# Kernel tuning notes

Measured on AMD Instinct MI355X. Metric: run time of the kernel, lower is better.

Reference implementation:

```python
import jax, jax.numpy as jnp
import numpy as np

N_USERS = 100000
N_MOVIES = 50000
EMB_DIM = 64
N_EDGES = 5000000


def setup_inputs() -> dict:
    key = jax.random.key(0)
    k1, k2, k3 = jax.random.split(key, 3)
    N = N_USERS + N_MOVIES
    edge_index = jax.random.randint(k1, (2, N_EDGES), 0, N, dtype=jnp.int64)
    user_emb = 0.1 * jax.random.normal(k2, (N_USERS, EMB_DIM), dtype=jnp.float32)
    movie_emb = 0.1 * jax.random.normal(k3, (N_MOVIES, EMB_DIM), dtype=jnp.float32)
    return {"edge_index": edge_index, "n_layers": 3,
            "user_emb": user_emb, "movie_emb": movie_emb}


def reference(edge_index, n_layers, user_emb, movie_emb):
    n_users = user_emb.shape[0]
    N = n_users + movie_emb.shape[0]
    x = jnp.concatenate([user_emb, movie_emb], axis=0)  # [N, D]

    row, col = edge_index[0], edge_index[1]  # source -> target
    # gcn_norm without self-loops (LGConv default): deg from target (col)
    deg = jnp.zeros((N,), x.dtype).at[col].add(1.0)
    dis = jnp.where(deg > 0, jax.lax.rsqrt(jnp.maximum(deg, 1.0)), 0.0)
    norm = dis[row] * dis[col]  # [E]

    acc = x
    total = x
    for _ in range(n_layers):
        msg = acc[row] * norm[:, None]            # [E, D] gather + scale
        acc = jax.ops.segment_sum(msg, col, num_segments=N)  # scatter-add
        total = total + acc
    final = total / (n_layers + 1)                # mean over layers 0..K
    return final[:n_users], final[n_users:]
```

## Files before the change

kernel.cpp:

```cpp
#include <hip/hip_runtime.h>

typedef _Float16 half_t;
typedef _Float16 half2_t __attribute__((ext_vector_type(2)));
union pk_u { unsigned int u; half2_t h; };

#define EMB 64
#define NLAYERS 3
#define BSH2 9
#define BW2 512
#define NB2MAX 512
#define GSPREAD 32
#define CAP 20480
#define EGCAP 34816
#define P1_BATCH 4096
#define P1_TH 512
#define P1_EPT 8
#define BINTH 1024

__device__ inline void scan_512w(const int* __restrict__ in, int* __restrict__ lstart,
                                 int* __restrict__ pair) {
    int t = threadIdx.x;
    int a0 = 0, a1 = 0;
    if (t < 256) { a0 = in[2 * t]; a1 = in[2 * t + 1]; pair[t] = a0 + a1; }
    __syncthreads();
    for (int off = 1; off < 256; off <<= 1) {
        int u = 0;
        if (t < 256 && t >= off) u = pair[t - off];
        __syncthreads();
        if (t < 256) pair[t] += u;
        __syncthreads();
    }
    if (t < 256) {
        lstart[2 * t]     = pair[t] - a0 - a1;
        lstart[2 * t + 1] = pair[t] - a1;
    }
    __syncthreads();
}

__global__ __launch_bounds__(512) void part_kernel(
        const int* __restrict__ row, const int* __restrict__ col,
        int* __restrict__ gcount, int* __restrict__ tmp, int E, int nb2) {
    __shared__ int hist[NB2MAX];
    __shared__ int lstart[NB2MAX];
    __shared__ int gbase[NB2MAX];
    __shared__ int pair[256];
    __shared__ int srec[P1_BATCH];
    __shared__ unsigned short sbuck[P1_BATCH];

    int base = blockIdx.x * P1_BATCH;
    int nE = min(P1_BATCH, E - base);

    for (int i = threadIdx.x; i < NB2MAX; i += P1_TH) hist[i] = 0;
    __syncthreads();

    int myc[P1_EPT];
    #pragma unroll
    for (int k = 0; k < P1_EPT; ++k) {
        int idx = base + (k << 9) + threadIdx.x;
        int c = (idx < E) ? col[idx] : -1;
        myc[k] = c;
        if (c >= 0) atomicAdd(&hist[c >> BSH2], 1);
    }
    __syncthreads();

    scan_512w(hist, lstart, pair);

    for (int b = threadIdx.x; b < nb2; b += P1_TH) {
        int c = hist[b];
        int off = 0;
        if (c > 0) off = atomicAdd(&gcount[b * GSPREAD], c);
        gbase[b] = b * CAP + off - lstart[b];
    }
    __syncthreads();
    for (int b = threadIdx.x; b < NB2MAX; b += P1_TH) hist[b] = lstart[b];
    __syncthreads();

    #pragma unroll
    for (int k = 0; k < P1_EPT; ++k) {
        int idx = base + (k << 9) + threadIdx.x;
        if (idx < E) {
            int c = myc[k];
            int b = c >> BSH2;
            int r = row[idx];
            int pos = atomicAdd(&hist[b], 1);
            srec[pos] = (r << BSH2) | (c & (BW2 - 1));
            sbuck[pos] = (unsigned short)b;
        }
    }
    __syncthreads();

    for (int i = threadIdx.x; i < nE; i += P1_TH)
        tmp[gbase[sbuck[i]] + i] = srec[i];
}

__global__ __launch_bounds__(1024) void bin_kernel(
        const int* __restrict__ tmp, const int* __restrict__ gcount,
        int* __restrict__ eg, int2* __restrict__ sd, float* __restrict__ dis,
        const float4* __restrict__ uev, const float4* __restrict__ mev,
        uint2* __restrict__ s0v,
        int n_users, int N) {
    __shared__ int hist[BW2];
    __shared__ int padh[BW2];
    __shared__ int lstart[BW2];
    __shared__ int pair[256];
    __shared__ float sdis[BW2];
    int b = blockIdx.x;
    int cnt = gcount[b * GSPREAD];
    int rbase = b * CAP;
    int ebase = b * EGCAP;
    int c0 = b << BSH2;
    int nc = min(BW2, N - c0);
    int sent = N << 7;

    for (int i = threadIdx.x; i < BW2; i += BINTH) hist[i] = 0;
    __syncthreads();
    for (int i = threadIdx.x; i < cnt; i += BINTH)
        atomicAdd(&hist[tmp[rbase + i] & (BW2 - 1)], 1);
    __syncthreads();

    for (int c = threadIdx.x; c < BW2; c += BINTH)
        padh[c] = (hist[c] + 63) & ~63;
    __syncthreads();

    scan_512w(padh, lstart, pair);

    for (int c = threadIdx.x; c < nc; c += BINTH) {
        int d = hist[c];
        float dn = (d > 0) ? rsqrtf((float)d) : 0.0f;
        sd[c0 + c] = make_int2(ebase + lstart[c], padh[c]);
        dis[c0 + c] = dn;
        sdis[c] = dn;
    }
    __syncthreads();
    for (int i = threadIdx.x; i < BW2; i += BINTH) hist[i] = lstart[i];
    __syncthreads();

    for (int i = threadIdx.x; i < cnt; i += BINTH) {
        int v = tmp[rbase + i];
        int pos = atomicAdd(&hist[v & (BW2 - 1)], 1);
        eg[ebase + pos] = (v >> BSH2) << 7;
    }
    __syncthreads();

    for (int c = threadIdx.x; c < nc; c += BINTH) {
        int en = lstart[c] + padh[c];
        for (int ppos = hist[c]; ppos < en; ++ppos) eg[ebase + ppos] = sent;
    }

    for (int i = threadIdx.x; i < nc * 16; i += BINTH) {
        int loc = i >> 4;
        int node = c0 + loc;
        int q = i & 15;
        const float4* src = (node < n_users) ? (uev + (long long)node * 16)
                                             : (mev + (long long)(node - n_users) * 16);
        float4 v = src[q];
        float dn = sdis[loc];
        pk_u w0, w1;
        w0.h[0] = (half_t)(v.x * dn); w0.h[1] = (half_t)(v.y * dn);
        w1.h[0] = (half_t)(v.z * dn); w1.h[1] = (half_t)(v.w * dn);
        s0v[(long long)node * 16 + q] = make_uint2(w0.u, w1.u);
    }
}

template <int LAYER>
__global__ __launch_bounds__(256) void gather_kernel(
        const int* __restrict__ eg, const int2* __restrict__ sd,
        const float* __restrict__ dis,
        const uint4* __restrict__ tab, uint2* __restrict__ sOut,
        uint2* __restrict__ uOut,
        const uint2* __restrict__ u1, const uint2* __restrict__ u2,
        const float4* __restrict__ uev, const float4* __restrict__ mev,
        float4* __restrict__ outv, int n_users, int N) {
    int wave = blockIdx.x * (blockDim.x >> 6) + (threadIdx.x >> 6);
    if (wave >= N) return;
    int l = threadIdx.x & 63;
    int p = l & 7;
    int h = l >> 3;
    unsigned pb = (unsigned)p << 4;
    const char* tb = (const char*)tab;

    int2 se = sd[wave];
    int j = se.x;
    int e = se.x + se.y;
    pk_u a0, a1, a2, a3;
    a0.u = 0; a1.u = 0; a2.u = 0; a3.u = 0;

    for (; j < e; j += 64) {
        int r0 = eg[j + h];
        int r1 = eg[j + 8 + h];
        int r2 = eg[j + 16 + h];
        int r3 = eg[j + 24 + h];
        int r4 = eg[j + 32 + h];
        int r5 = eg[j + 40 + h];
        int r6 = eg[j + 48 + h];
        int r7 = eg[j + 56 + h];
        uint4 v0 = *(const uint4*)(tb + ((unsigned)r0 + pb));
        uint4 v1 = *(const uint4*)(tb + ((unsigned)r1 + pb));
        uint4 v2 = *(const uint4*)(tb + ((unsigned)r2 + pb));
        uint4 v3 = *(const uint4*)(tb + ((unsigned)r3 + pb));
        uint4 v4 = *(const uint4*)(tb + ((unsigned)r4 + pb));
        uint4 v5 = *(const uint4*)(tb + ((unsigned)r5 + pb));
        uint4 v6 = *(const uint4*)(tb + ((unsigned)r6 + pb));
        uint4 v7 = *(const uint4*)(tb + ((unsigned)r7 + pb));
        pk_u t;
        t.u = v0.x; a0.h += t.h; t.u = v0.y; a1.h += t.h;
        t.u = v0.z; a2.h += t.h; t.u = v0.w; a3.h += t.h;
        t.u = v1.x; a0.h += t.h; t.u = v1.y; a1.h += t.h;
        t.u = v1.z; a2.h += t.h; t.u = v1.w; a3.h += t.h;
        t.u = v2.x; a0.h += t.h; t.u = v2.y; a1.h += t.h;
        t.u = v2.z; a2.h += t.h; t.u = v2.w; a3.h += t.h;
        t.u = v3.x; a0.h += t.h; t.u = v3.y; a1.h += t.h;
        t.u = v3.z; a2.h += t.h; t.u = v3.w; a3.h += t.h;
        t.u = v4.x; a0.h += t.h; t.u = v4.y; a1.h += t.h;
        t.u = v4.z; a2.h += t.h; t.u = v4.w; a3.h += t.h;
        t.u = v5.x; a0.h += t.h; t.u = v5.y; a1.h += t.h;
        t.u = v5.z; a2.h += t.h; t.u = v5.w; a3.h += t.h;
        t.u = v6.x; a0.h += t.h; t.u = v6.y; a1.h += t.h;
        t.u = v6.z; a2.h += t.h; t.u = v6.w; a3.h += t.h;
        t.u = v7.x; a0.h += t.h; t.u = v7.y; a1.h += t.h;
        t.u = v7.z; a2.h += t.h; t.u = v7.w; a3.h += t.h;
    }

    #pragma unroll
    for (int m = 8; m <= 32; m <<= 1) {
        pk_u t;
        t.u = (unsigned int)__shfl_xor((int)a0.u, m); a0.h += t.h;
        t.u = (unsigned int)__shfl_xor((int)a1.u, m); a1.h += t.h;
        t.u = (unsigned int)__shfl_xor((int)a2.u, m); a2.h += t.h;
        t.u = (unsigned int)__shfl_xor((int)a3.u, m); a3.h += t.h;
    }

    if (h < 2) {
        pk_u x0 = h ? a2 : a0;
        pk_u x1 = h ? a3 : a1;
        float dc = dis[wave];
        float g0 = dc * (float)x0.h[0];
        float g1 = dc * (float)x0.h[1];
        float g2 = dc * (float)x1.h[0];
        float g3 = dc * (float)x1.h[1];
        int q = p * 2 + h;
        long long o16 = (long long)wave * 16 + q;
        if (LAYER < 3) {
            pk_u w0, w1, uw0, uw1;
            w0.h[0] = (half_t)(dc * g0); w0.h[1] = (half_t)(dc * g1);
            w1.h[0] = (half_t)(dc * g2); w1.h[1] = (half_t)(dc * g3);
            uw0.h[0] = (half_t)g0; uw0.h[1] = (half_t)g1;
            uw1.h[0] = (half_t)g2; uw1.h[1] = (half_t)g3;
            sOut[o16] = make_uint2(w0.u, w1.u);
            long long uo = (LAYER == 1) ? o16 : ((long long)wave * 32 + q);
            uOut[uo] = make_uint2(uw0.u, uw1.u);
        } else {
            const float4* src = (wave < n_users) ? (uev + (long long)wave * 16)
                                                 : (mev + (long long)(wave - n_users) * 16);
            float4 xv = src[q];
            uint2 ua2 = u1[o16];
            uint2 ub2 = u2[(long long)wave * 32 + q];
            pk_u pa, pb2, pc, pd;
            pa.u = ua2.x; pb2.u = ua2.y; pc.u = ub2.x; pd.u = ub2.y;
            float4 r;
            r.x = (xv.x + (float)pa.h[0]  + (float)pc.h[0] + g0) * 0.25f;
            r.y = (xv.y + (float)pa.h[1]  + (float)pc.h[1] + g1) * 0.25f;
            r.z = (xv.z + (float)pb2.h[0] + (float)pd.h[0] + g2) * 0.25f;
            r.w = (xv.w + (float)pb2.h[1] + (float)pd.h[1] + g3) * 0.25f;
            outv[o16] = r;
        }
    }
}

extern "C" void kernel_launch(void* const* d_in, const int* in_sizes, int n_in,
                              void* d_out, int out_size, void* d_ws, size_t ws_size,
                              hipStream_t stream) {
    const int*   edge = (const int*)d_in[0];
    const float* ue   = (const float*)d_in[2];
    const float* me   = (const float*)d_in[3];
    float*       out  = (float*)d_out;

    const int E        = in_sizes[0] / 2;
    const int n_users  = in_sizes[2] / EMB;
    const int n_movies = in_sizes[3] / EMB;
    const int N        = n_users + n_movies;
    const int* row = edge;
    const int* col = edge + E;
    const int nb2 = (N + BW2 - 1) >> BSH2;

    char* ws = (char*)d_ws;
    auto align_up = [](size_t v) { return (v + 255) & ~(size_t)255; };
    int*    gcount = (int*)ws;    ws += align_up((size_t)NB2MAX * GSPREAD * sizeof(int));
    int2*   sd     = (int2*)ws;   ws += align_up((size_t)N * sizeof(int2));
    float*  dis    = (float*)ws;  ws += align_up((size_t)N * sizeof(float));
    int*    tmp    = (int*)ws;    ws += align_up((size_t)nb2 * CAP * sizeof(int));
    int*    eg     = (int*)ws;    ws += align_up((size_t)nb2 * EGCAP * sizeof(int));
    half_t* sA     = (half_t*)ws; ws += align_up((size_t)(N + 1) * EMB * sizeof(half_t));
    half_t* sB     = (half_t*)ws; ws += align_up((size_t)(N + 1) * EMB * sizeof(half_t));
    uint2* u1 = (uint2*)tmp;
    uint2* u2 = (uint2*)out;

    hipMemsetAsync(gcount, 0, (size_t)NB2MAX * GSPREAD * sizeof(int), stream);
    hipMemsetAsync(sA + (size_t)N * EMB, 0, EMB * sizeof(half_t), stream);
    hipMemsetAsync(sB + (size_t)N * EMB, 0, EMB * sizeof(half_t), stream);
    part_kernel<<<(E + P1_BATCH - 1) / P1_BATCH, P1_TH, 0, stream>>>(
        row, col, gcount, tmp, E, nb2);
    bin_kernel<<<nb2, BINTH, 0, stream>>>(
        tmp, gcount, eg, sd, dis,
        (const float4*)ue, (const float4*)me, (uint2*)sA,
        n_users, N);

    const int waves_per_block = 4;
    const int gblocks = (N + waves_per_block - 1) / waves_per_block;
    gather_kernel<1><<<gblocks, 256, 0, stream>>>(
        eg, sd, dis, (const uint4*)sA, (uint2*)sB, u1,
        nullptr, nullptr, nullptr, nullptr, nullptr, n_users, N);
    gather_kernel<2><<<gblocks, 256, 0, stream>>>(
        eg, sd, dis, (const uint4*)sB, (uint2*)sA, u2,
        nullptr, nullptr, nullptr, nullptr, nullptr, n_users, N);
    gather_kernel<3><<<gblocks, 256, 0, stream>>>(
        eg, sd, dis, (const uint4*)sA, nullptr, nullptr,
        (const uint2*)u1, (const uint2*)u2,
        (const float4*)ue, (const float4*)me, (float4*)out, n_users, N);
}
```

Baseline: 487.7 us.

## Halve bucket width, pad edge lists to 32, and software-pipeline index loads in gather

Bucket width drops from 512 to 256 nodes, with per-node edge lists padded to multiples of 32 instead of 64. This cuts the sentinel padding edges that every layer gathers, which matters most for low-degree nodes. The gather loop now processes 32 edges per step and prefetches the next step's indices before gathering the current embeddings. Sentinel fill is spread across threads, and 64 extra sentinels are written past the end so the prefetch can read out of range safely. The cost is more buckets and partition histogram entries, and smaller per-iteration memory-level parallelism in the gather.

After: 486.0 us. About the same (-0.3%).

```diff
diff --git a/kernel.cpp b/kernel.cpp
--- a/kernel.cpp
+++ b/kernel.cpp
@@ -6,31 +6,33 @@
 
 #define EMB 64
 #define NLAYERS 3
-#define BSH2 9
-#define BW2 512
-#define NB2MAX 512
+#define BSH2 8
+#define BW2 256
+#define NB2MAX 1024
 #define GSPREAD 32
-#define CAP 20480
-#define EGCAP 34816
+#define CAP 10240
+#define EGCAP 16384
 #define P1_BATCH 4096
 #define P1_TH 512
 #define P1_EPT 8
-#define BINTH 1024
-
-__device__ inline void scan_512w(const int* __restrict__ in, int* __restrict__ lstart,
+#define BINTH 512
+
+template <int NE>
+__device__ inline void scan_pow2(const int* __restrict__ in, int* __restrict__ lstart,
                                  int* __restrict__ pair) {
+    const int H = NE / 2;
     int t = threadIdx.x;
     int a0 = 0, a1 = 0;
-    if (t < 256) { a0 = in[2 * t]; a1 = in[2 * t + 1]; pair[t] = a0 + a1; }
-    __syncthreads();
-    for (int off = 1; off < 256; off <<= 1) {
+    if (t < H) { a0 = in[2 * t]; a1 = in[2 * t + 1]; pair[t] = a0 + a1; }
+    __syncthreads();
+    for (int off = 1; off < H; off <<= 1) {
         int u = 0;
-        if (t < 256 && t >= off) u = pair[t - off];
+        if (t < H && t >= off) u = pair[t - off];
         __syncthreads();
-        if (t < 256) pair[t] += u;
+        if (t < H) pair[t] += u;
         __syncthreads();
     }
-    if (t < 256) {
+    if (t < H) {
         lstart[2 * t]     = pair[t] - a0 - a1;
         lstart[2 * t + 1] = pair[t] - a1;
     }
@@ -43,7 +45,7 @@
     __shared__ int hist[NB2MAX];
     __shared__ int lstart[NB2MAX];
     __shared__ int gbase[NB2MAX];
-    __shared__ int pair[256];
+    __shared__ int pair[NB2MAX / 2];
     __shared__ int srec[P1_BATCH];
     __shared__ unsigned short sbuck[P1_BATCH];
 
@@ -63,7 +65,7 @@
     }
     __syncthreads();
 
-    scan_512w(hist, lstart, pair);
+    scan_pow2<NB2MAX>(hist, lstart, pair);
 
     for (int b = threadIdx.x; b < nb2; b += P1_TH) {
         int c = hist[b];
@@ -93,7 +95,7 @@
         tmp[gbase[sbuck[i]] + i] = srec[i];
 }
 
-__global__ __launch_bounds__(1024) void bin_kernel(
+__global__ __launch_bounds__(512) void bin_kernel(
         const int* __restrict__ tmp, const int* __restrict__ gcount,
         int* __restrict__ eg, int2* __restrict__ sd, float* __restrict__ dis,
         const float4* __restrict__ uev, const float4* __restrict__ mev,
@@ -102,7 +104,7 @@
     __shared__ int hist[BW2];
     __shared__ int padh[BW2];
     __shared__ int lstart[BW2];
-    __shared__ int pair[256];
+    __shared__ int pair[BW2 / 2];
     __shared__ float sdis[BW2];
     int b = blockIdx.x;
     int cnt = gcount[b * GSPREAD];
@@ -119,10 +121,10 @@
     __syncthreads();
 
     for (int c = threadIdx.x; c < BW2; c += BINTH)
-        padh[c] = (hist[c] + 63) & ~63;
-    __syncthreads();
-
-    scan_512w(padh, lstart, pair);
+        padh[c] = (hist[c] + 31) & ~31;
+    __syncthreads();
+
+    scan_pow2<BW2>(padh, lstart, pair);
 
     for (int c = threadIdx.x; c < nc; c += BINTH) {
         int d = hist[c];
@@ -142,10 +144,15 @@
     }
     __syncthreads();
 
-    for (int c = threadIdx.x; c < nc; c += BINTH) {
+    for (int i = threadIdx.x; i < BW2 * 32; i += BINTH) {
+        int c = i >> 5;
+        int o = i & 31;
+        int st = hist[c];
         int en = lstart[c] + padh[c];
-        for (int ppos = hist[c]; ppos < en; ++ppos) eg[ebase + ppos] = sent;
-    }
+        if (st + o < en) eg[ebase + st + o] = sent;
+    }
+    int tot = lstart[BW2 - 1] + padh[BW2 - 1];
+    if (threadIdx.x < 64) eg[ebase + tot + threadIdx.x] = sent;
 
     for (int i = threadIdx.x; i < nc * 16; i += BINTH) {
         int loc = i >> 4;
@@ -185,40 +192,31 @@
     pk_u a0, a1, a2, a3;
     a0.u = 0; a1.u = 0; a2.u = 0; a3.u = 0;
 
-    for (; j < e; j += 64) {
+    if (j < e) {
         int r0 = eg[j + h];
         int r1 = eg[j + 8 + h];
         int r2 = eg[j + 16 + h];
         int r3 = eg[j + 24 + h];
-        int r4 = eg[j + 32 + h];
-        int r5 = eg[j + 40 + h];
-        int r6 = eg[j + 48 + h];
-        int r7 = eg[j + 56 + h];
-        uint4 v0 = *(const uint4*)(tb + ((unsigned)r0 + pb));
-        uint4 v1 = *(const uint4*)(tb + ((unsigned)r1 + pb));
-        uint4 v2 = *(const uint4*)(tb + ((unsigned)r2 + pb));
-        uint4 v3 = *(const uint4*)(tb + ((unsigned)r3 + pb));
-        uint4 v4 = *(const uint4*)(tb + ((unsigned)r4 + pb));
-        uint4 v5 = *(const uint4*)(tb + ((unsigned)r5 + pb));
-        uint4 v6 = *(const uint4*)(tb + ((unsigned)r6 + pb));
-        uint4 v7 = *(const uint4*)(tb + ((unsigned)r7 + pb));
-        pk_u t;
-        t.u = v0.x; a0.h += t.h; t.u = v0.y; a1.h += t.h;
-        t.u = v0.z; a2.h += t.h; t.u = v0.w; a3.h += t.h;
-        t.u = v1.x; a0.h += t.h; t.u = v1.y; a1.h += t.h;
-        t.u = v1.z; a2.h += t.h; t.u = v1.w; a3.h += t.h;
-        t.u = v2.x; a0.h += t.h; t.u = v2.y; a1.h += t.h;
-        t.u = v2.z; a2.h += t.h; t.u = v2.w; a3.h += t.h;
-        t.u = v3.x; a0.h += t.h; t.u = v3.y; a1.h += t.h;
-        t.u = v3.z; a2.h += t.h; t.u = v3.w; a3.h += t.h;
-        t.u = v4.x; a0.h += t.h; t.u = v4.y; a1.h += t.h;
-        t.u = v4.z; a2.h += t.h; t.u = v4.w; a3.h += t.h;
-        t.u = v5.x; a0.h += t.h; t.u = v5.y; a1.h += t.h;
-        t.u = v5.z; a2.h += t.h; t.u = v5.w; a3.h += t.h;
-        t.u = v6.x; a0.h += t.h; t.u = v6.y; a1.h += t.h;
-        t.u = v6.z; a2.h += t.h; t.u = v6.w; a3.h += t.h;
-        t.u = v7.x; a0.h += t.h; t.u = v7.y; a1.h += t.h;
-        t.u = v7.z; a2.h += t.h; t.u = v7.w; a3.h += t.h;
+        for (; j < e; j += 32) {
+            int n0 = eg[j + 32 + h];
+            int n1 = eg[j + 40 + h];
+            int n2 = eg[j + 48 + h];
+            int n3 = eg[j + 56 + h];
+            uint4 v0 = *(const uint4*)(tb + ((unsigned)r0 + pb));
+            uint4 v1 = *(const uint4*)(tb + ((unsigned)r1 + pb));
+            uint4 v2 = *(const uint4*)(tb + ((unsigned)r2 + pb));
+            uint4 v3 = *(const uint4*)(tb + ((unsigned)r3 + pb));
+            pk_u t;
+            t.u = v0.x; a0.h += t.h; t.u = v0.y; a1.h += t.h;
+            t.u = v0.z; a2.h += t.h; t.u = v0.w; a3.h += t.h;
+            t.u = v1.x; a0.h += t.h; t.u = v1.y; a1.h += t.h;
+            t.u = v1.z; a2.h += t.h; t.u = v1.w; a3.h += t.h;
+            t.u = v2.x; a0.h += t.h; t.u = v2.y; a1.h += t.h;
+            t.u = v2.z; a2.h += t.h; t.u = v2.w; a3.h += t.h;
+            t.u = v3.x; a0.h += t.h; t.u = v3.y; a1.h += t.h;
+            t.u = v3.z; a2.h += t.h; t.u = v3.w; a3.h += t.h;
+            r0 = n0; r1 = n1; r2 = n2; r3 = n3;
+        }
     }
 
     #pragma unroll
```
